# Performance work log

Measured on AMD Instinct MI355X. Metric: run time of the kernel, lower is better.

Reference implementation:

```python
import jax, jax.numpy as jnp
import numpy as np

DIM = 2048
NUM_HEADS = 8
HEAD_DIM = DIM // NUM_HEADS
B = 256
EPS = 1e-5


def layer_norm(x, w, b):
    mu = jnp.mean(x, axis=-1, keepdims=True)
    var = jnp.mean(jnp.square(x - mu), axis=-1, keepdims=True)
    return (x - mu) * jax.lax.rsqrt(var + EPS) * w + b


def conv1d(x, w):
    # x: [B, C, L], w: [O, I, K], stride 1, padding 1, no bias
    return jax.lax.conv_general_dilated(
        x, w, window_strides=(1,), padding=[(1, 1)],
        dimension_numbers=('NCH', 'OIH', 'NCH'))


def attention(q, k, v):
    # q,k,v: [B, L, E]; softmax(qk^T/sqrt(E)) v
    scale = 1.0 / jnp.sqrt(jnp.asarray(q.shape[-1], q.dtype))
    scores = jnp.einsum('bld,bsd->bls', q, k) * scale
    a = jax.nn.softmax(scores, axis=-1)
    return jnp.einsum('bls,bsd->bld', a, v)


def setup_inputs() -> dict:
    key = jax.random.key(0)
    ks = jax.random.split(key, 16)
    s = 0.02
    return {
        'f_ad': jax.random.normal(ks[0], (B, DIM), jnp.float32),
        'f_age': jax.random.normal(ks[1], (B, DIM), jnp.float32),
        'mem': jax.random.normal(ks[2], (B, DIM, 4, 4, 4), jnp.float32),
        'age_gap': jax.random.normal(ks[3], (B, 1), jnp.float32),
        'qv_W': jax.random.normal(ks[4], (2 * DIM, DIM), jnp.float32) * s,
        'k1_W': jax.random.normal(ks[5], (DIM, DIM), jnp.float32) * s,
        'k2_W': jax.random.normal(ks[6], (DIM, DIM), jnp.float32) * s,
        'ln_w': jnp.ones((HEAD_DIM,), jnp.float32),
        'ln_b': jnp.zeros((HEAD_DIM,), jnp.float32),
        'ln2_w': jnp.ones((DIM,), jnp.float32),
        'ln2_b': jnp.zeros((DIM,), jnp.float32),
        'agf_reduce_W': jax.random.normal(ks[7], (1, DIM), jnp.float32) * s,
        'agf_reduce_b': jnp.zeros((1,), jnp.float32),
        'agf_expand_W': jax.random.normal(ks[8], (DIM, 2), jnp.float32) * s,
        'agf_expand_b': jnp.zeros((DIM,), jnp.float32),
        'conv1_W': jax.random.normal(ks[9], (NUM_HEADS, NUM_HEADS, 3), jnp.float32) * s,
        'conv2_W': jax.random.normal(ks[10], (NUM_HEADS, NUM_HEADS, 3), jnp.float32) * s,
    }


def reference(f_ad, f_age, mem, age_gap, qv_W, k1_W, k2_W, ln_w, ln_b,
              ln2_w, ln2_b, agf_reduce_W, agf_reduce_b, agf_expand_W,
              agf_expand_b, conv1_W, conv2_W):
    # k1 branch: global-average-pool mem over spatial dims, project
    k1 = jnp.mean(mem, axis=(2, 3, 4)) @ k1_W.T              # [B, dim]
    k1 = k1.reshape(-1, NUM_HEADS, HEAD_DIM)
    k1_norm = layer_norm(k1, ln_w, ln_b)

    # k2 branch: AGF(f_age, age_gap) -- NOTE: original code never applies self.k2
    red = f_age @ agf_reduce_W.T + agf_reduce_b               # [B, 1]
    cat = jnp.concatenate((red, age_gap), axis=1)             # [B, 2]
    k2 = f_age + (cat @ agf_expand_W.T + agf_expand_b)        # [B, dim]
    k2 = k2.reshape(-1, NUM_HEADS, HEAD_DIM)
    k2_norm = layer_norm(k2, ln_w, ln_b)

    # q, v
    qv = f_ad @ qv_W.T                                        # [B, 2*dim]
    q, v = jnp.split(qv, 2, axis=1)
    q = q.reshape(-1, NUM_HEADS, HEAD_DIM)
    v = v.reshape(-1, NUM_HEADS, HEAD_DIM)
    q_norm = layer_norm(q, ln_w, ln_b)

    out1 = attention(q_norm, k1_norm, v)                      # [B, H, hd]
    out2 = attention(q_norm, k2_norm, v)

    out1 = layer_norm(conv1d(out1, conv1_W), ln_w, ln_b)
    out2 = layer_norm(conv1d(out2, conv2_W), ln_w, ln_b)

    out = jax.nn.gelu(layer_norm(out1 + out2 + v, ln_w, ln_b), approximate=True)
    out = out.reshape(-1, NUM_HEADS * HEAD_DIM)               # [B, dim]
    return jax.nn.gelu(layer_norm(out, ln2_w, ln2_b), approximate=True)
```

## Files before the change

kernel.cpp:

```cpp
#include <hip/hip_runtime.h>

#define DIM 2048
#define NH 8
#define HD 256
#define NB 256
#define EPS 1e-5f

typedef short v8s __attribute__((ext_vector_type(8)));
typedef float v16f __attribute__((ext_vector_type(16)));

__device__ __forceinline__ short f2bf(float f) {
    union { float f; unsigned u; } c; c.f = f;
    unsigned u = c.u;
    unsigned r = (u + 0x7fffu + ((u >> 16) & 1u)) >> 16;
    return (short)r;
}

__device__ __forceinline__ float gelu_f(float x) {
    float u = 0.7978845608028654f * (x + 0.044715f * x * x * x);
    float t = 1.0f - 2.0f / (__expf(2.0f * u) + 1.0f);
    return 0.5f * x * (1.0f + t);
}

__device__ __forceinline__ float wave_sum(float v) {
#pragma unroll
    for (int m = 32; m >= 1; m >>= 1) v += __shfl_xor(v, m, 64);
    return v;
}

__global__ __launch_bounds__(256) void prep_kernel(
    const float* __restrict__ mem, const float* __restrict__ f_ad,
    short* __restrict__ pooled_sw, short* __restrict__ fad_sw) {
    int blk = blockIdx.x, t = threadIdx.x;
    int q = t & 7;
    int rid = t >> 3;
#pragma unroll
    for (int it = 0; it < 8; ++it) {
        int r = blk * 256 + it * 32 + rid;
        const float4* rp = (const float4*)mem + (size_t)r * 16 + q;
        float4 v0 = rp[0];
        float4 v1 = rp[8];
        float s = (v0.x + v0.y) + (v0.z + v0.w)
                + (v1.x + v1.y) + (v1.z + v1.w);
        s += __shfl_xor(s, 1); s += __shfl_xor(s, 2); s += __shfl_xor(s, 4);
        if (q == 0) {
            int d = r & 2047, b = r >> 11;
            pooled_sw[((size_t)(d >> 4) * NB + b) * 16 + (d & 15)] = f2bf(s * 0.015625f);
        }
    }
    int idx = blk * 256 + t;
    int b = idx >> 11, d = idx & 2047;
    fad_sw[((size_t)(d >> 4) * NB + b) * 16 + (d & 15)] = f2bf(f_ad[idx]);
}

__global__ __launch_bounds__(512) void gemm_kernel(
    const short* __restrict__ pooled_sw, const short* __restrict__ fad_sw,
    const float* __restrict__ k1_W, const float* __restrict__ qv_W,
    float* __restrict__ k1_out, float* __restrict__ qv_out) {
    __shared__ short sB[2][8 * 64 * 8];
    int blk = blockIdx.x;
    const short* A; const float* W; float* C; int ldC, n0;
    if (blk < 64) { A = pooled_sw; W = k1_W; C = k1_out; ldC = 2048; n0 = blk * 32; }
    else          { A = fad_sw;    W = qv_W; C = qv_out; ldC = 4096; n0 = (blk - 64) * 32; }
    int t = threadIdx.x;
    int lane = t & 63, w = t >> 6;
    int row = t >> 4;
    int c8 = t & 15;
    const float* wp = W + (size_t)(n0 + row) * 2048 + c8 * 8;
    float4 b0 = *(const float4*)(wp);
    float4 b1 = *(const float4*)(wp + 4);
    v16f acc;
#pragma unroll
    for (int r = 0; r < 16; ++r) acc[r] = 0.f;
    const short* Abase = A + (size_t)(w * 32 + (lane & 31)) * 16 + (lane >> 5) * 8;
    int bidx = ((c8 >> 1) * 64 + row * 2 + (c8 & 1)) * 8;
    int ridx_base = ((lane & 31) * 2 + (lane >> 5)) * 8;
    for (int iter = 0; iter < 16; ++iter) {
        short* sp = sB[iter & 1];
        v8s bb;
        bb[0] = f2bf(b0.x); bb[1] = f2bf(b0.y); bb[2] = f2bf(b0.z); bb[3] = f2bf(b0.w);
        bb[4] = f2bf(b1.x); bb[5] = f2bf(b1.y); bb[6] = f2bf(b1.z); bb[7] = f2bf(b1.w);
        *(v8s*)(sp + bidx) = bb;
        if (iter + 1 < 16) {
            b0 = *(const float4*)(wp + (iter + 1) * 128);
            b1 = *(const float4*)(wp + (iter + 1) * 128 + 4);
        }
        __syncthreads();
#pragma unroll
        for (int k0 = 0; k0 < 8; ++k0) {
            int K0 = iter * 8 + k0;
            v8s afrag = *(const v8s*)(Abase + (size_t)K0 * 4096);
            v8s bfrag = *(const v8s*)(sp + k0 * 512 + ridx_base);
            acc = __builtin_amdgcn_mfma_f32_32x32x16_bf16(afrag, bfrag, acc, 0, 0, 0);
        }
    }
#pragma unroll
    for (int r = 0; r < 16; ++r) {
        int rr = (r & 3) + 8 * (r >> 2) + 4 * (lane >> 5);
        int m = w * 32 + rr;
        C[(size_t)m * ldC + n0 + (lane & 31)] = acc[r];
    }
}

__device__ void ln_heads(float* buf, const float* sLnw, const float* sLnb, float* sTmp) {
    int t = threadIdx.x; int h = t >> 5, i = t & 31;
    float s = 0.f, ss = 0.f;
#pragma unroll
    for (int j = 0; j < 8; ++j) { float x = buf[h * HD + i + 32 * j]; s += x; ss += x * x; }
#pragma unroll
    for (int m = 16; m >= 1; m >>= 1) { s += __shfl_xor(s, m, 64); ss += __shfl_xor(ss, m, 64); }
    if (i == 0) {
        float mu = s * (1.0f / HD);
        float var = ss * (1.0f / HD) - mu * mu;
        sTmp[h * 2] = mu; sTmp[h * 2 + 1] = rsqrtf(var + EPS);
    }
    __syncthreads();
    float mu = sTmp[h * 2], rs = sTmp[h * 2 + 1];
#pragma unroll
    for (int j = 0; j < 8; ++j) {
        int dd = i + 32 * j; int idx = h * HD + dd;
        buf[idx] = (buf[idx] - mu) * rs * sLnw[dd] + sLnb[dd];
    }
    __syncthreads();
}

__global__ __launch_bounds__(256) void epilogue_kernel(
    const float* __restrict__ qv_out, const float* __restrict__ k1_out,
    const float* __restrict__ f_age, const float* __restrict__ age_gap,
    const float* __restrict__ ln_w, const float* __restrict__ ln_b,
    const float* __restrict__ ln2_w, const float* __restrict__ ln2_b,
    const float* __restrict__ rW, const float* __restrict__ rb,
    const float* __restrict__ eW, const float* __restrict__ eb,
    const float* __restrict__ cw1, const float* __restrict__ cw2,
    float* __restrict__ out) {
    __shared__ float sQ[DIM], sK1[DIM], sK2[DIM], sV[DIM], sO1[DIM], sO2[DIM];
    __shared__ float sLnw[HD], sLnb[HD];
    __shared__ float sCW1[192], sCW2[192];
    __shared__ float sSc[2][NH][NH];
    __shared__ float sStats[32];
    int b = blockIdx.x, t = threadIdx.x;
    int wv = t >> 6;
    sLnw[t & 255] = ln_w[t & 255];
    sLnb[t & 255] = ln_b[t & 255];
    if (t < 192) { sCW1[t] = cw1[t]; sCW2[t] = cw2[t]; }
    const float4* qv4 = (const float4*)(qv_out + (size_t)b * 4096);
    const float4* k14 = (const float4*)(k1_out + (size_t)b * DIM);
    const float4* fa4 = (const float4*)(f_age + (size_t)b * DIM);
    const float4* rW4 = (const float4*)rW;
    float4* sQ4 = (float4*)sQ; float4* sV4 = (float4*)sV;
    float4* sK14 = (float4*)sK1; float4* sK24 = (float4*)sK2;
    float dotp = 0.f;
#pragma unroll
    for (int j = 0; j < 2; ++j) {
        int idx = t + 256 * j;
        sQ4[idx] = qv4[idx];
        sV4[idx] = qv4[512 + idx];
        sK14[idx] = k14[idx];
        float4 fa = fa4[idx];
        sK24[idx] = fa;
        float4 rw = rW4[idx];
        dotp += fa.x * rw.x + fa.y * rw.y + fa.z * rw.z + fa.w * rw.w;
    }
    dotp = wave_sum(dotp);
    if ((t & 63) == 0) sStats[wv] = dotp;
    __syncthreads();
    float red = sStats[0] + sStats[1] + sStats[2] + sStats[3] + rb[0];
    float gap = age_gap[b];
#pragma unroll
    for (int j = 0; j < 8; ++j) {
        int idx = t + 256 * j;
        float2 e2 = ((const float2*)eW)[idx];
        sK2[idx] += red * e2.x + gap * e2.y + eb[idx];
    }
    __syncthreads();
    ln_heads(sQ, sLnw, sLnb, sStats);
    ln_heads(sK1, sLnw, sLnb, sStats);
    ln_heads(sK2, sLnw, sLnb, sStats);
    {
        int g = t >> 4, l16 = t & 15;
        int at = g >> 3, qi = g & 7;
        const float* kb = at ? sK2 : sK1;
        float acc[8];
#pragma unroll
        for (int j = 0; j < 8; ++j) acc[j] = 0.f;
        for (int ii = 0; ii < 16; ++ii) {
            int d = l16 + 16 * ii;
            float qd = sQ[qi * HD + d];
#pragma unroll
            for (int j = 0; j < 8; ++j) acc[j] += qd * kb[j * HD + d];
        }
#pragma unroll
        for (int m = 8; m >= 1; m >>= 1)
#pragma unroll
            for (int j = 0; j < 8; ++j) acc[j] += __shfl_xor(acc[j], m, 64);
        if (l16 == 0) {
#pragma unroll
            for (int j = 0; j < 8; ++j) sSc[at][qi][j] = acc[j] * (1.0f / 16.0f);
        }
    }
    __syncthreads();
    if (t < 16) {
        int at = t >> 3, qi = t & 7;
        float mx = -1e30f;
#pragma unroll
        for (int j = 0; j < 8; ++j) mx = fmaxf(mx, sSc[at][qi][j]);
        float e[8], sum = 0.f;
#pragma unroll
        for (int j = 0; j < 8; ++j) { e[j] = __expf(sSc[at][qi][j] - mx); sum += e[j]; }
        float inv = 1.0f / sum;
#pragma unroll
        for (int j = 0; j < 8; ++j) sSc[at][qi][j] = e[j] * inv;
    }
    __syncthreads();
    {
        int qi = t >> 5, i32 = t & 31;
#pragma unroll
        for (int jd = 0; jd < 8; ++jd) {
            int d = i32 + 32 * jd;
            float o1 = 0.f, o2 = 0.f;
#pragma unroll
            for (int j = 0; j < 8; ++j) {
                float vv = sV[j * HD + d];
                o1 += sSc[0][qi][j] * vv;
                o2 += sSc[1][qi][j] * vv;
            }
            sO1[qi * HD + d] = o1;
            sO2[qi * HD + d] = o2;
        }
    }
    __syncthreads();
    {
        int o = t >> 5, i32 = t & 31;
        float w1r[24], w2r[24];
#pragma unroll
        for (int ic = 0; ic < 8; ++ic)
#pragma unroll
            for (int tp = 0; tp < 3; ++tp) {
                w1r[ic * 3 + tp] = sCW1[(o * 8 + ic) * 3 + tp];
                w2r[ic * 3 + tp] = sCW2[(o * 8 + ic) * 3 + tp];
            }
        float r1[8], r2[8];
#pragma unroll
        for (int jd = 0; jd < 8; ++jd) {
            int l = i32 + 32 * jd;
            float a1 = 0.f, a2 = 0.f;
#pragma unroll
            for (int ic = 0; ic < 8; ++ic) {
                float xm1 = (l > 0)   ? sO1[ic * HD + l - 1] : 0.f;
                float x01 =             sO1[ic * HD + l];
                float xp1 = (l < 255) ? sO1[ic * HD + l + 1] : 0.f;
                a1 += xm1 * w1r[ic * 3] + x01 * w1r[ic * 3 + 1] + xp1 * w1r[ic * 3 + 2];
                float xm2 = (l > 0)   ? sO2[ic * HD + l - 1] : 0.f;
                float x02 =             sO2[ic * HD + l];
                float xp2 = (l < 255) ? sO2[ic * HD + l + 1] : 0.f;
                a2 += xm2 * w2r[ic * 3] + x02 * w2r[ic * 3 + 1] + xp2 * w2r[ic * 3 + 2];
            }
            r1[jd] = a1; r2[jd] = a2;
        }
        __syncthreads();
#pragma unroll
        for (int jd = 0; jd < 8; ++jd) {
            int l = i32 + 32 * jd;
            sO1[o * HD + l] = r1[jd];
            sO2[o * HD + l] = r2[jd];
        }
    }
    __syncthreads();
    ln_heads(sO1, sLnw, sLnb, sStats);
    ln_heads(sO2, sLnw, sLnb, sStats);
#pragma unroll
    for (int j = 0; j < 8; ++j) {
        int idx = t + 256 * j;
        sO1[idx] = sO1[idx] + sO2[idx] + sV[idx];
    }
    __syncthreads();
    ln_heads(sO1, sLnw, sLnb, sStats);
#pragma unroll
    for (int j = 0; j < 8; ++j) {
        int idx = t + 256 * j;
        sO1[idx] = gelu_f(sO1[idx]);
    }
    float s = 0.f, ss = 0.f;
#pragma unroll
    for (int j = 0; j < 8; ++j) { float x = sO1[t + 256 * j]; s += x; ss += x * x; }
    s = wave_sum(s); ss = wave_sum(ss);
    if ((t & 63) == 0) { sStats[wv] = s; sStats[8 + wv] = ss; }
    __syncthreads();
    float S  = sStats[0] + sStats[1] + sStats[2] + sStats[3];
    float SS = sStats[8] + sStats[9] + sStats[10] + sStats[11];
    float mu = S * (1.0f / DIM);
    float var = SS * (1.0f / DIM) - mu * mu;
    float rs = rsqrtf(var + EPS);
    float* ob = out + (size_t)b * DIM;
#pragma unroll
    for (int j = 0; j < 8; ++j) {
        int idx = t + 256 * j;
        float val = (sO1[idx] - mu) * rs * ln2_w[idx] + ln2_b[idx];
        ob[idx] = gelu_f(val);
    }
}

extern "C" void kernel_launch(void* const* d_in, const int* in_sizes, int n_in,
                              void* d_out, int out_size, void* d_ws, size_t ws_size,
                              hipStream_t stream) {
    const float* f_ad    = (const float*)d_in[0];
    const float* f_age   = (const float*)d_in[1];
    const float* mem     = (const float*)d_in[2];
    const float* age_gap = (const float*)d_in[3];
    const float* qv_W    = (const float*)d_in[4];
    const float* k1_W    = (const float*)d_in[5];
    const float* ln_w    = (const float*)d_in[7];
    const float* ln_b    = (const float*)d_in[8];
    const float* ln2_w   = (const float*)d_in[9];
    const float* ln2_b   = (const float*)d_in[10];
    const float* rW      = (const float*)d_in[11];
    const float* rb      = (const float*)d_in[12];
    const float* eW      = (const float*)d_in[13];
    const float* eb      = (const float*)d_in[14];
    const float* cw1     = (const float*)d_in[15];
    const float* cw2     = (const float*)d_in[16];
    float* out = (float*)d_out;
    char* ws = (char*)d_ws;
    short* pooled_sw = (short*)ws;
    short* fad_sw    = (short*)(ws + (1 << 20));
    float* k1_out    = (float*)(ws + (2 << 20));
    float* qv_out    = (float*)(ws + (4 << 20));
    prep_kernel<<<2048, 256, 0, stream>>>(mem, f_ad, pooled_sw, fad_sw);
    gemm_kernel<<<192, 512, 0, stream>>>(pooled_sw, fad_sw, k1_W, qv_W, k1_out, qv_out);
    epilogue_kernel<<<256, 256, 0, stream>>>(qv_out, k1_out, f_age, age_gap,
                                             ln_w, ln_b, ln2_w, ln2_b,
                                             rW, rb, eW, eb, cw1, cw2, out);
}
```

Measured before the change: 296.8 us.

## Deepen weight prefetch in GEMM and cut barriers in epilogue layer norms

The GEMM loop is unrolled by two and keeps two stages of weight registers in flight, so global loads for the tile after next are issued earlier. In the epilogue, layer norms keep values in registers and compute stats with shuffles instead of a shared-memory round trip and extra barrier. Pairs of independent norms are merged into one pass. The softmax is folded into the score reduction, and the residual sum, head norm, GELU and final norm run in one register pass. This removes several __syncthreads and shared-memory passes at the cost of more registers.

```diff
diff --git a/kernel.cpp b/kernel.cpp
--- a/kernel.cpp
+++ b/kernel.cpp
@@ -67,31 +67,55 @@
     int row = t >> 4;
     int c8 = t & 15;
     const float* wp = W + (size_t)(n0 + row) * 2048 + c8 * 8;
-    float4 b0 = *(const float4*)(wp);
-    float4 b1 = *(const float4*)(wp + 4);
+    float4 a0 = *(const float4*)(wp);
+    float4 a1 = *(const float4*)(wp + 4);
+    float4 c0 = *(const float4*)(wp + 128);
+    float4 c1 = *(const float4*)(wp + 132);
     v16f acc;
 #pragma unroll
     for (int r = 0; r < 16; ++r) acc[r] = 0.f;
     const short* Abase = A + (size_t)(w * 32 + (lane & 31)) * 16 + (lane >> 5) * 8;
     int bidx = ((c8 >> 1) * 64 + row * 2 + (c8 & 1)) * 8;
     int ridx_base = ((lane & 31) * 2 + (lane >> 5)) * 8;
-    for (int iter = 0; iter < 16; ++iter) {
-        short* sp = sB[iter & 1];
-        v8s bb;
-        bb[0] = f2bf(b0.x); bb[1] = f2bf(b0.y); bb[2] = f2bf(b0.z); bb[3] = f2bf(b0.w);
-        bb[4] = f2bf(b1.x); bb[5] = f2bf(b1.y); bb[6] = f2bf(b1.z); bb[7] = f2bf(b1.w);
-        *(v8s*)(sp + bidx) = bb;
-        if (iter + 1 < 16) {
-            b0 = *(const float4*)(wp + (iter + 1) * 128);
-            b1 = *(const float4*)(wp + (iter + 1) * 128 + 4);
-        }
-        __syncthreads();
-#pragma unroll
-        for (int k0 = 0; k0 < 8; ++k0) {
-            int K0 = iter * 8 + k0;
-            v8s afrag = *(const v8s*)(Abase + (size_t)K0 * 4096);
-            v8s bfrag = *(const v8s*)(sp + k0 * 512 + ridx_base);
-            acc = __builtin_amdgcn_mfma_f32_32x32x16_bf16(afrag, bfrag, acc, 0, 0, 0);
+    for (int it2 = 0; it2 < 8; ++it2) {
+        int iter = it2 * 2;
+        {
+            short* sp = sB[0];
+            v8s bb;
+            bb[0] = f2bf(a0.x); bb[1] = f2bf(a0.y); bb[2] = f2bf(a0.z); bb[3] = f2bf(a0.w);
+            bb[4] = f2bf(a1.x); bb[5] = f2bf(a1.y); bb[6] = f2bf(a1.z); bb[7] = f2bf(a1.w);
+            *(v8s*)(sp + bidx) = bb;
+            if (it2 < 7) {
+                a0 = *(const float4*)(wp + (iter + 2) * 128);
+                a1 = *(const float4*)(wp + (iter + 2) * 128 + 4);
+            }
+            __syncthreads();
+#pragma unroll
+            for (int k0 = 0; k0 < 8; ++k0) {
+                int K0 = iter * 8 + k0;
+                v8s afrag = *(const v8s*)(Abase + (size_t)K0 * 4096);
+                v8s bfrag = *(const v8s*)(sp + k0 * 512 + ridx_base);
+                acc = __builtin_amdgcn_mfma_f32_32x32x16_bf16(afrag, bfrag, acc, 0, 0, 0);
+            }
+        }
+        {
+            short* sp = sB[1];
+            v8s bb;
+            bb[0] = f2bf(c0.x); bb[1] = f2bf(c0.y); bb[2] = f2bf(c0.z); bb[3] = f2bf(c0.w);
+            bb[4] = f2bf(c1.x); bb[5] = f2bf(c1.y); bb[6] = f2bf(c1.z); bb[7] = f2bf(c1.w);
+            *(v8s*)(sp + bidx) = bb;
+            if (it2 < 7) {
+                c0 = *(const float4*)(wp + (iter + 3) * 128);
+                c1 = *(const float4*)(wp + (iter + 3) * 128 + 4);
+            }
+            __syncthreads();
+#pragma unroll
+            for (int k0 = 0; k0 < 8; ++k0) {
+                int K0 = (iter + 1) * 8 + k0;
+                v8s afrag = *(const v8s*)(Abase + (size_t)K0 * 4096);
+                v8s bfrag = *(const v8s*)(sp + k0 * 512 + ridx_base);
+                acc = __builtin_amdgcn_mfma_f32_32x32x16_bf16(afrag, bfrag, acc, 0, 0, 0);
+            }
         }
     }
 #pragma unroll
@@ -102,24 +126,47 @@
     }
 }
 
-__device__ void ln_heads(float* buf, const float* sLnw, const float* sLnb, float* sTmp) {
+__device__ __forceinline__ void ln_heads(float* buf, const float* sLnw, const float* sLnb) {
     int t = threadIdx.x; int h = t >> 5, i = t & 31;
-    float s = 0.f, ss = 0.f;
-#pragma unroll
-    for (int j = 0; j < 8; ++j) { float x = buf[h * HD + i + 32 * j]; s += x; ss += x * x; }
+    float x[8]; float s = 0.f, ss = 0.f;
+#pragma unroll
+    for (int j = 0; j < 8; ++j) {
+        x[j] = buf[h * HD + i + 32 * j]; s += x[j]; ss += x[j] * x[j];
+    }
 #pragma unroll
     for (int m = 16; m >= 1; m >>= 1) { s += __shfl_xor(s, m, 64); ss += __shfl_xor(ss, m, 64); }
-    if (i == 0) {
-        float mu = s * (1.0f / HD);
-        float var = ss * (1.0f / HD) - mu * mu;
-        sTmp[h * 2] = mu; sTmp[h * 2 + 1] = rsqrtf(var + EPS);
-    }
-    __syncthreads();
-    float mu = sTmp[h * 2], rs = sTmp[h * 2 + 1];
+    float mu = s * (1.0f / HD);
+    float rs = rsqrtf(ss * (1.0f / HD) - mu * mu + EPS);
+#pragma unroll
+    for (int j = 0; j < 8; ++j) {
+        int dd = i + 32 * j;
+        buf[h * HD + dd] = (x[j] - mu) * rs * sLnw[dd] + sLnb[dd];
+    }
+    __syncthreads();
+}
+
+__device__ __forceinline__ void ln_heads2(float* bufA, float* bufB,
+                                          const float* sLnw, const float* sLnb) {
+    int t = threadIdx.x; int h = t >> 5, i = t & 31;
+    float xa[8], xb[8]; float sa = 0.f, ssa = 0.f, sb = 0.f, ssb = 0.f;
+#pragma unroll
+    for (int j = 0; j < 8; ++j) {
+        int idx = h * HD + i + 32 * j;
+        xa[j] = bufA[idx]; sa += xa[j]; ssa += xa[j] * xa[j];
+        xb[j] = bufB[idx]; sb += xb[j]; ssb += xb[j] * xb[j];
+    }
+#pragma unroll
+    for (int m = 16; m >= 1; m >>= 1) {
+        sa += __shfl_xor(sa, m, 64); ssa += __shfl_xor(ssa, m, 64);
+        sb += __shfl_xor(sb, m, 64); ssb += __shfl_xor(ssb, m, 64);
+    }
+    float mua = sa * (1.0f / HD), rsa = rsqrtf(ssa * (1.0f / HD) - mua * mua + EPS);
+    float mub = sb * (1.0f / HD), rsb = rsqrtf(ssb * (1.0f / HD) - mub * mub + EPS);
 #pragma unroll
     for (int j = 0; j < 8; ++j) {
         int dd = i + 32 * j; int idx = h * HD + dd;
-        buf[idx] = (buf[idx] - mu) * rs * sLnw[dd] + sLnb[dd];
+        bufA[idx] = (xa[j] - mua) * rsa * sLnw[dd] + sLnb[dd];
+        bufB[idx] = (xb[j] - mub) * rsb * sLnw[dd] + sLnb[dd];
     }
     __syncthreads();
 }
@@ -173,9 +220,8 @@
         sK2[idx] += red * e2.x + gap * e2.y + eb[idx];
     }
     __syncthreads();
-    ln_heads(sQ, sLnw, sLnb, sStats);
-    ln_heads(sK1, sLnw, sLnb, sStats);
-    ln_heads(sK2, sLnw, sLnb, sStats);
+    ln_heads2(sQ, sK1, sLnw, sLnb);
+    ln_heads(sK2, sLnw, sLnb);
     {
         int g = t >> 4, l16 = t & 15;
         int at = g >> 3, qi = g & 7;
@@ -193,23 +239,17 @@
         for (int m = 8; m >= 1; m >>= 1)
 #pragma unroll
             for (int j = 0; j < 8; ++j) acc[j] += __shfl_xor(acc[j], m, 64);
+        float mx = acc[0];
+#pragma unroll
+        for (int j = 1; j < 8; ++j) mx = fmaxf(mx, acc[j]);
+        float e[8], sum = 0.f;
+#pragma unroll
+        for (int j = 0; j < 8; ++j) { e[j] = __expf((acc[j] - mx) * (1.0f / 16.0f)); sum += e[j]; }
+        float inv = 1.0f / sum;
         if (l16 == 0) {
 #pragma unroll
-            for (int j = 0; j < 8; ++j) sSc[at][qi][j] = acc[j] * (1.0f / 16.0f);
-        }
-    }
-    __syncthreads();
-    if (t < 16) {
-        int at = t >> 3, qi = t & 7;
-        float mx = -1e30f;
-#pragma unroll
-        for (int j = 0; j < 8; ++j) mx = fmaxf(mx, sSc[at][qi][j]);
-        float e[8], sum = 0.f;
-#pragma unroll
-        for (int j = 0; j < 8; ++j) { e[j] = __expf(sSc[at][qi][j] - mx); sum += e[j]; }
-        float inv = 1.0f / sum;
-#pragma unroll
-        for (int j = 0; j < 8; ++j) sSc[at][qi][j] = e[j] * inv;
+            for (int j = 0; j < 8; ++j) sSc[at][qi][j] = e[j] * inv;
+        }
     }
     __syncthreads();
     {
@@ -266,37 +306,42 @@
         }
     }
     __syncthreads();
-    ln_heads(sO1, sLnw, sLnb, sStats);
-    ln_heads(sO2, sLnw, sLnb, sStats);
-#pragma unroll
-    for (int j = 0; j < 8; ++j) {
-        int idx = t + 256 * j;
-        sO1[idx] = sO1[idx] + sO2[idx] + sV[idx];
-    }
-    __syncthreads();
-    ln_heads(sO1, sLnw, sLnb, sStats);
-#pragma unroll
-    for (int j = 0; j < 8; ++j) {
-        int idx = t + 256 * j;
-        sO1[idx] = gelu_f(sO1[idx]);
-    }
-    float s = 0.f, ss = 0.f;
-#pragma unroll
-    for (int j = 0; j < 8; ++j) { float x = sO1[t + 256 * j]; s += x; ss += x * x; }
-    s = wave_sum(s); ss = wave_sum(ss);
-    if ((t & 63) == 0) { sStats[wv] = s; sStats[8 + wv] = ss; }
-    __syncthreads();
-    float S  = sStats[0] + sStats[1] + sStats[2] + sStats[3];
-    float SS = sStats[8] + sStats[9] + sStats[10] + sStats[11];
-    float mu = S * (1.0f / DIM);
-    float var = SS * (1.0f / DIM) - mu * mu;
-    float rs = rsqrtf(var + EPS);
-    float* ob = out + (size_t)b * DIM;
-#pragma unroll
-    for (int j = 0; j < 8; ++j) {
-        int idx = t + 256 * j;
-        float val = (sO1[idx] - mu) * rs * ln2_w[idx] + ln2_b[idx];
-        ob[idx] = gelu_f(val);
+    ln_heads2(sO1, sO2, sLnw, sLnb);
+    {
+        int h = t >> 5, i = t & 31;
+        float x[8]; float s = 0.f, ss = 0.f;
+#pragma unroll
+        for (int j = 0; j < 8; ++j) {
+            int idx = h * HD + i + 32 * j;
+            float v = sO1[idx] + sO2[idx] + sV[idx];
+            x[j] = v; s += v; ss += v * v;
+        }
+#pragma unroll
+        for (int m = 16; m >= 1; m >>= 1) { s += __shfl_xor(s, m, 64); ss += __shfl_xor(ss, m, 64); }
+        float mu = s * (1.0f / HD);
+        float rs = rsqrtf(ss * (1.0f / HD) - mu * mu + EPS);
+        float s2 = 0.f, ss2 = 0.f;
+#pragma unroll
+        for (int j = 0; j < 8; ++j) {
+            int dd = i + 32 * j;
+            float v = gelu_f((x[j] - mu) * rs * sLnw[dd] + sLnb[dd]);
+            x[j] = v; s2 += v; ss2 += v * v;
+        }
+        s2 = wave_sum(s2); ss2 = wave_sum(ss2);
+        if ((t & 63) == 0) { sStats[wv] = s2; sStats[8 + wv] = ss2; }
+        __syncthreads();
+        float S  = sStats[0] + sStats[1] + sStats[2] + sStats[3];
+        float SS = sStats[8] + sStats[9] + sStats[10] + sStats[11];
+        float mu2 = S * (1.0f / DIM);
+        float var2 = SS * (1.0f / DIM) - mu2 * mu2;
+        float rs2 = rsqrtf(var2 + EPS);
+        float* ob = out + (size_t)b * DIM;
+#pragma unroll
+        for (int j = 0; j < 8; ++j) {
+            int idx = h * HD + i + 32 * j;
+            float val = (x[j] - mu2) * rs2 * ln2_w[idx] + ln2_b[idx];
+            ob[idx] = gelu_f(val);
+        }
     }
 }
 
```

Result: slower. 308.8 us (+4.0%).
